# Kernel tuning notes

Measured on AMD Instinct MI355X. Metric: run time of the kernel, lower is better.

## Reference

```python
import jax, jax.numpy as jnp
import numpy as np

N_NODES = 50000


def gcn_conv(x, W, b, src, dst):
    # PyG GCNConv: h = x @ W; add self-loops; norm = deg^{-1/2}[src]*deg^{-1/2}[dst];
    # out = scatter_add(norm * h[src] -> dst) + bias
    h = x @ W  # [N, out]
    ones = jnp.ones(src.shape[0], dtype=x.dtype)
    deg = jax.ops.segment_sum(ones, dst, num_segments=N_NODES) + 1.0  # +1 for self-loop
    inv_sqrt = deg ** -0.5
    norm = inv_sqrt[src] * inv_sqrt[dst]  # [E]
    msgs = h[src] * norm[:, None]  # [E, out]
    agg = jax.ops.segment_sum(msgs, dst, num_segments=N_NODES)
    # self-loop contribution: norm_ii = deg_i^{-1}
    agg = agg + h * (inv_sqrt * inv_sqrt)[:, None]
    return agg + b


def setup_inputs() -> dict:
    key = jax.random.key(0)
    k1, k2, k3, k4 = jax.random.split(key, 4)
    d_in, d_h = 256, 256
    x = jax.random.normal(k1, (N_NODES, d_in), dtype=jnp.float32)
    edge_index = jax.random.randint(k2, (2, 800000), 0, N_NODES, dtype=jnp.int64)
    # Glorot-style params (GCNConv linear has no bias; separate bias added post-agg)
    W1 = jax.random.normal(k3, (d_in, d_h), dtype=jnp.float32) / np.sqrt(d_in)
    W2 = jax.random.normal(k4, (d_h, d_h), dtype=jnp.float32) / np.sqrt(d_h)
    b1 = jnp.zeros((d_h,), dtype=jnp.float32)
    b2 = jnp.zeros((d_h,), dtype=jnp.float32)
    return {"x": x, "edge_index": edge_index, "W1": W1, "b1": b1, "W2": W2, "b2": b2}


def reference(x, edge_index, W1, b1, W2, b2):
    src, dst = edge_index[0], edge_index[1]
    h = jax.nn.relu(gcn_conv(x, W1, b1, src, dst))
    h = jax.nn.relu(gcn_conv(h, W2, b2, src, dst))
    # global_mean_pool with batch=arange(N) assigns each node its own graph -> identity
    return h
```

## Files before the change

### kernel.cpp

```cpp
#include <hip/hip_runtime.h>
#include <hip/hip_bf16.h>

typedef unsigned short u16;
typedef unsigned int u32;

#define N_NODES 50000
#define N_EDGES 800000
#define DHID 256
#define ELLW 64

typedef __attribute__((ext_vector_type(8))) _Float16 f16x8;
typedef __attribute__((ext_vector_type(4))) float f32x4;
typedef __attribute__((ext_vector_type(2))) float f32x2;

__device__ __forceinline__ u16 f2bf(float f) {
    u32 u = __float_as_uint(f);
    u32 r = (u + 0x7FFFu + ((u >> 16) & 1u)) >> 16;
    return (u16)r;
}
__device__ __forceinline__ u16 f2h(float f) {
    _Float16 h = (_Float16)f;
    union { _Float16 h; u16 u; } c; c.h = h;
    return c.u;
}
__device__ __forceinline__ void gl_lds16(const void* g, void* l) {
    __builtin_amdgcn_global_load_lds(
        (const __attribute__((address_space(1))) u32*)g,
        (__attribute__((address_space(3))) u32*)l, 16, 0, 0);
}

#define SPLIT_BLKS 12500
#define ZERO_BLKS 196
__global__ void prep_fused(const float* __restrict__ x, u16* __restrict__ xf,
                           const float* __restrict__ W1, const float* __restrict__ W2,
                           u16* __restrict__ W1t, u16* __restrict__ W2t,
                           int* __restrict__ deg, u32* __restrict__ hszero) {
    const int b = blockIdx.x, tid = threadIdx.x;
    if (b < SPLIT_BLKS) {
        int i = b * 256 + tid;
        float4 v = ((const float4*)x)[i];
        u16 h0 = f2h(v.x), h1 = f2h(v.y), h2 = f2h(v.z), h3 = f2h(v.w);
        uint2 hv;
        hv.x = (u32)h0 | ((u32)h1 << 16);
        hv.y = (u32)h2 | ((u32)h3 << 16);
        ((uint2*)xf)[i] = hv;
    } else if (b < SPLIT_BLKS + ZERO_BLKS) {
        int j = (b - SPLIT_BLKS) * 256 + tid;
        if (j < N_NODES) deg[j] = 0;
        if (j < 128) hszero[j] = 0;
    } else {
        int idx = b - (SPLIT_BLKS + ZERO_BLKS);
        int y = idx >> 8, n = idx & 255, k = tid;
        const float* W = y ? W2 : W1;
        u16* o = y ? W2t : W1t;
        o[n * 256 + k] = f2h(W[k * 256 + n]);
    }
}

__global__ void fill_kernel(const int* __restrict__ src, const int* __restrict__ dst,
                            int* __restrict__ deg, u16* __restrict__ col16, int E) {
    int e = blockIdx.x * 256 + threadIdx.x;
    if (e < E) {
        int d = dst[e];
        int p = atomicAdd(&deg[d], 1);
        if (p < ELLW) col16[(size_t)d * ELLW + p] = (u16)src[e];
    }
}

__global__ __launch_bounds__(256) void gemm_f16_kernel(
    const u16* __restrict__ Af, const u16* __restrict__ Bt,
    const int* __restrict__ deg, u16* __restrict__ out, int M) {
    __shared__ u16 As[2][128 * 32];
    __shared__ u16 Bs[2][128 * 32];
    const int tid = threadIdx.x;
    const int wave = tid >> 6;
    const int lane = tid & 63;
    const int wm = wave >> 1, wn = wave & 1;
    const int quad = lane >> 4, l16 = lane & 15;
    const int m0 = blockIdx.x * 128;
    const int n0 = blockIdx.y * 128;

    f32x4 acc[4][4] = {};

    const int rl = tid >> 2;
    const int cl = tid & 3;
    const int kk = ((cl ^ (rl & 3) ^ ((rl >> 2) & 3)) & 3) * 8;
    int ar0 = m0 + rl; if (ar0 >= M) ar0 = M - 1;
    int ar1 = m0 + 64 + rl; if (ar1 >= M) ar1 = M - 1;
    const size_t aoff0 = (size_t)ar0 * 256 + kk;
    const size_t aoff1 = (size_t)ar1 * 256 + kk;
    const size_t boff0 = (size_t)(n0 + rl) * 256 + kk;
    const size_t boff1 = (size_t)(n0 + 64 + rl) * 256 + kk;
    const size_t l0 = (size_t)wave * 512;
    const size_t l1 = 2048 + (size_t)wave * 512;

    const int qs8 = ((quad ^ (l16 & 3) ^ ((l16 >> 2) & 3)) & 3) * 8;

#define STAGE(buf, ko)                                      \
    {                                                       \
        const int koff_ = (ko) * 32;                        \
        gl_lds16(Af + aoff0 + koff_, &As[buf][l0]);         \
        gl_lds16(Af + aoff1 + koff_, &As[buf][l1]);         \
        gl_lds16(Bt + boff0 + koff_, &Bs[buf][l0]);         \
        gl_lds16(Bt + boff1 + koff_, &Bs[buf][l1]);         \
    }

    STAGE(0, 0);
    asm volatile("s_waitcnt vmcnt(0)" ::: "memory");
    __syncthreads();

    int cur = 0;
    for (int ko = 0; ko < 8; ++ko) {
        if (ko < 7) STAGE(cur ^ 1, ko + 1);

        f16x8 af[4], bf[4];
#pragma unroll
        for (int mi = 0; mi < 4; ++mi)
            af[mi] = *(const f16x8*)&As[cur][(wm * 64 + mi * 16 + l16) * 32 + qs8];
#pragma unroll
        for (int ni = 0; ni < 4; ++ni)
            bf[ni] = *(const f16x8*)&Bs[cur][(wn * 64 + ni * 16 + l16) * 32 + qs8];
#pragma unroll
        for (int mi = 0; mi < 4; ++mi)
#pragma unroll
            for (int ni = 0; ni < 4; ++ni)
                acc[mi][ni] = __builtin_amdgcn_mfma_f32_16x16x32_f16(af[mi], bf[ni], acc[mi][ni], 0, 0, 0);

        if (ko < 7) {
            asm volatile("s_waitcnt vmcnt(0)" ::: "memory");
            __syncthreads();
            cur ^= 1;
        }
    }
#undef STAGE

#pragma unroll
    for (int mi = 0; mi < 4; ++mi) {
#pragma unroll
        for (int r = 0; r < 4; ++r) {
            int row = m0 + wm * 64 + mi * 16 + quad * 4 + r;
            if (row < M) {
                float s = rsqrtf((float)deg[row] + 1.0f);
#pragma unroll
                for (int ni = 0; ni < 4; ++ni) {
                    int c = n0 + wn * 64 + ni * 16 + l16;
                    out[(size_t)row * 256 + c] = f2bf(acc[mi][ni][r] * s);
                }
            }
        }
    }
}

__global__ __launch_bounds__(256) void agg_kernel(
    const u16* __restrict__ hs, const u16* __restrict__ col16,
    const int* __restrict__ deg, const float* __restrict__ bias,
    u16* __restrict__ out_f16, float* __restrict__ out_f,
    int mode, int Nn) {
    const int wave = threadIdx.x >> 6, lane = threadIdx.x & 63;
    const int i = blockIdx.x * 4 + wave;
    if (i >= Nn) return;

    const int cnt = deg[i];
    const size_t ebase = (size_t)i * ELLW;
    int entry = Nn;
    if (lane == 0) entry = i;
    else if (lane - 1 < cnt) entry = (int)col16[ebase + lane - 1];
    int entries = cnt + 1;
    if (entries > 64) entries = 64;
    const int nb = (entries + 3) >> 2;
    const size_t lofs = (size_t)lane * 4;

    f32x2 a01 = {0.f, 0.f}, a23 = {0.f, 0.f};

#define ISSUE(b, x0, x1, x2, x3)                                                \
    {                                                                           \
        int e0 = __builtin_amdgcn_readlane(entry, (b) * 4 + 0);                 \
        int e1 = __builtin_amdgcn_readlane(entry, (b) * 4 + 1);                 \
        int e2 = __builtin_amdgcn_readlane(entry, (b) * 4 + 2);                 \
        int e3 = __builtin_amdgcn_readlane(entry, (b) * 4 + 3);                 \
        x0 = *(const uint2*)(hs + (size_t)e0 * 256 + lofs);                     \
        x1 = *(const uint2*)(hs + (size_t)e1 * 256 + lofs);                     \
        x2 = *(const uint2*)(hs + (size_t)e2 * 256 + lofs);                     \
        x3 = *(const uint2*)(hs + (size_t)e3 * 256 + lofs);                     \
    }
#define ACCUM(v)                                                                \
    {                                                                           \
        f32x2 p0, p1;                                                           \
        p0.x = __uint_as_float(v.x << 16);                                      \
        p0.y = __uint_as_float(v.x & 0xffff0000u);                              \
        p1.x = __uint_as_float(v.y << 16);                                      \
        p1.y = __uint_as_float(v.y & 0xffff0000u);                              \
        a01 += p0; a23 += p1;                                                   \
    }

    uint2 c0, c1, c2, c3, d0, d1, d2, d3, n0v, n1v, n2v, n3v;
    ISSUE(0, c0, c1, c2, c3);
    if (nb > 1) ISSUE(1, d0, d1, d2, d3);
    for (int b = 0; b < nb; ++b) {
        const bool more2 = (b + 2 < nb);
        if (more2) ISSUE(b + 2, n0v, n1v, n2v, n3v);
        ACCUM(c0); ACCUM(c1); ACCUM(c2); ACCUM(c3);
        c0 = d0; c1 = d1; c2 = d2; c3 = d3;
        d0 = n0v; d1 = n1v; d2 = n2v; d3 = n3v;
    }
    {
        int cap = cnt < ELLW ? cnt : ELLW;
        for (int j = 63; j < cap; ++j) {
            int s = (int)col16[ebase + j];
            uint2 v = *(const uint2*)(hs + (size_t)s * 256 + lofs);
            ACCUM(v);
        }
    }
#undef ISSUE
#undef ACCUM

    const float inv = rsqrtf((float)cnt + 1.0f);
    float4 bb = *(const float4*)(bias + lane * 4);
    float r0 = fmaxf(fmaf(a01.x, inv, bb.x), 0.0f);
    float r1 = fmaxf(fmaf(a01.y, inv, bb.y), 0.0f);
    float r2 = fmaxf(fmaf(a23.x, inv, bb.z), 0.0f);
    float r3 = fmaxf(fmaf(a23.y, inv, bb.w), 0.0f);
    const size_t o = (size_t)i * 256 + lane * 4;
    if (mode == 0) {
        u16 h0 = f2h(r0), h1 = f2h(r1), h2 = f2h(r2), h3 = f2h(r3);
        uint2 w;
        w.x = (u32)h0 | ((u32)h1 << 16);
        w.y = (u32)h2 | ((u32)h3 << 16);
        *(uint2*)(out_f16 + o) = w;
    } else {
        *(float4*)(out_f + o) = make_float4(r0, r1, r2, r3);
    }
}

extern "C" void kernel_launch(void* const* d_in, const int* in_sizes, int n_in,
                              void* d_out, int out_size, void* d_ws, size_t ws_size,
                              hipStream_t stream) {
    const float* x = (const float*)d_in[0];
    const int* ei = (const int*)d_in[1];
    const float* W1 = (const float*)d_in[2];
    const float* b1 = (const float*)d_in[3];
    const float* W2 = (const float*)d_in[4];
    const float* b2 = (const float*)d_in[5];
    float* out = (float*)d_out;

    const int Nn = N_NODES, E = N_EDGES;
    const int* srcp = ei;
    const int* dstp = ei + E;

    u16* Af = (u16*)d_out;

    char* p = (char*)d_ws;
    auto take = [&](size_t bytes) -> void* {
        void* r = (void*)p;
        p += (bytes + 255) & ~(size_t)255;
        return r;
    };
    u16* hs    = (u16*)take((size_t)(Nn + 1) * DHID * 2);
    u16* col16 = (u16*)take((size_t)Nn * ELLW * 2);
    int* deg   = (int*)take((size_t)Nn * 4);
    u16* W1t   = (u16*)take(256 * 256 * 2);
    u16* W2t   = (u16*)take(256 * 256 * 2);

    prep_fused<<<SPLIT_BLKS + ZERO_BLKS + 512, 256, 0, stream>>>(
        x, Af, W1, W2, W1t, W2t, deg, (u32*)(hs + (size_t)Nn * DHID));
    fill_kernel<<<E / 256, 256, 0, stream>>>(srcp, dstp, deg, col16, E);

    const int gm = (Nn + 127) / 128;
    gemm_f16_kernel<<<dim3(gm, 2), 256, 0, stream>>>(Af, W1t, deg, hs, Nn);
    agg_kernel<<<(Nn + 3) / 4, 256, 0, stream>>>(hs, col16, deg, b1, Af, nullptr, 0, Nn);
    gemm_f16_kernel<<<dim3(gm, 2), 256, 0, stream>>>(Af, W2t, deg, hs, Nn);
    agg_kernel<<<(Nn + 3) / 4, 256, 0, stream>>>(hs, col16, deg, b2, nullptr, out, 1, Nn);
}
```

Baseline: 308.5 us.

## Slice hidden features into 32-column panels for cache-local aggregation

The GEMM now writes its bf16 output in a sliced layout: 8 slices of 32 columns, each a contiguous [N+1, 32] array. The aggregation kernel assigns each block to one slice and 16 nodes, so each gather reads 64-byte rows from a smaller working set that should fit better in cache. The zero-fill now runs as its own kernel, and the edge-fill work is merged into the prep kernel. One risk is that merging fill into prep lets the fill atomics run concurrently with other prep blocks. Another is that the aggregation loop becomes fully unrolled with shuffles, and each lane now issues narrower 4-byte loads.

```diff
diff --git a/kernel.cpp b/kernel.cpp
--- a/kernel.cpp
+++ b/kernel.cpp
@@ -8,10 +8,11 @@
 #define N_EDGES 800000
 #define DHID 256
 #define ELLW 64
+#define NSLICE 8
+#define SLICEW 32
 
 typedef __attribute__((ext_vector_type(8))) _Float16 f16x8;
 typedef __attribute__((ext_vector_type(4))) float f32x4;
-typedef __attribute__((ext_vector_type(2))) float f32x2;
 
 __device__ __forceinline__ u16 f2bf(float f) {
     u32 u = __float_as_uint(f);
@@ -29,12 +30,23 @@
         (__attribute__((address_space(3))) u32*)l, 16, 0, 0);
 }
 
+__global__ void zero_kernel(int* __restrict__ deg, u32* __restrict__ hss32) {
+    int j = blockIdx.x * 256 + threadIdx.x;
+    if (j < N_NODES) deg[j] = 0;
+    if (j < NSLICE * 16) {
+        int s = j >> 4, w = j & 15;
+        hss32[((size_t)s * (N_NODES + 1) + N_NODES) * 16 + w] = 0;
+    }
+}
+
 #define SPLIT_BLKS 12500
-#define ZERO_BLKS 196
-__global__ void prep_fused(const float* __restrict__ x, u16* __restrict__ xf,
-                           const float* __restrict__ W1, const float* __restrict__ W2,
-                           u16* __restrict__ W1t, u16* __restrict__ W2t,
-                           int* __restrict__ deg, u32* __restrict__ hszero) {
+#define W_BLKS 512
+#define FILL_BLKS 3125
+__global__ void prep_fill(const float* __restrict__ x, u16* __restrict__ xf,
+                          const float* __restrict__ W1, const float* __restrict__ W2,
+                          u16* __restrict__ W1t, u16* __restrict__ W2t,
+                          const int* __restrict__ src, const int* __restrict__ dst,
+                          int* __restrict__ deg, u16* __restrict__ col16) {
     const int b = blockIdx.x, tid = threadIdx.x;
     if (b < SPLIT_BLKS) {
         int i = b * 256 + tid;
@@ -44,23 +56,14 @@
         hv.x = (u32)h0 | ((u32)h1 << 16);
         hv.y = (u32)h2 | ((u32)h3 << 16);
         ((uint2*)xf)[i] = hv;
-    } else if (b < SPLIT_BLKS + ZERO_BLKS) {
-        int j = (b - SPLIT_BLKS) * 256 + tid;
-        if (j < N_NODES) deg[j] = 0;
-        if (j < 128) hszero[j] = 0;
-    } else {
-        int idx = b - (SPLIT_BLKS + ZERO_BLKS);
+    } else if (b < SPLIT_BLKS + W_BLKS) {
+        int idx = b - SPLIT_BLKS;
         int y = idx >> 8, n = idx & 255, k = tid;
         const float* W = y ? W2 : W1;
         u16* o = y ? W2t : W1t;
         o[n * 256 + k] = f2h(W[k * 256 + n]);
-    }
-}
-
-__global__ void fill_kernel(const int* __restrict__ src, const int* __restrict__ dst,
-                            int* __restrict__ deg, u16* __restrict__ col16, int E) {
-    int e = blockIdx.x * 256 + threadIdx.x;
-    if (e < E) {
+    } else {
+        int e = (b - SPLIT_BLKS - W_BLKS) * 256 + tid;
         int d = dst[e];
         int p = atomicAdd(&deg[d], 1);
         if (p < ELLW) col16[(size_t)d * ELLW + p] = (u16)src[e];
@@ -69,7 +72,7 @@
 
 __global__ __launch_bounds__(256) void gemm_f16_kernel(
     const u16* __restrict__ Af, const u16* __restrict__ Bt,
-    const int* __restrict__ deg, u16* __restrict__ out, int M) {
+    const int* __restrict__ deg, u16* __restrict__ hss, int M) {
     __shared__ u16 As[2][128 * 32];
     __shared__ u16 Bs[2][128 * 32];
     const int tid = threadIdx.x;
@@ -144,7 +147,8 @@
 #pragma unroll
                 for (int ni = 0; ni < 4; ++ni) {
                     int c = n0 + wn * 64 + ni * 16 + l16;
-                    out[(size_t)row * 256 + c] = f2bf(acc[mi][ni][r] * s);
+                    size_t o = ((size_t)(c >> 5) * (N_NODES + 1) + row) * 32 + (c & 31);
+                    hss[o] = f2bf(acc[mi][ni][r] * s);
                 }
             }
         }
@@ -152,83 +156,67 @@
 }
 
 __global__ __launch_bounds__(256) void agg_kernel(
-    const u16* __restrict__ hs, const u16* __restrict__ col16,
+    const u16* __restrict__ hss, const u16* __restrict__ col16,
     const int* __restrict__ deg, const float* __restrict__ bias,
     u16* __restrict__ out_f16, float* __restrict__ out_f,
     int mode, int Nn) {
+    const int slice = blockIdx.x & 7;
+    const int chunk = blockIdx.x >> 3;
     const int wave = threadIdx.x >> 6, lane = threadIdx.x & 63;
-    const int i = blockIdx.x * 4 + wave;
-    if (i >= Nn) return;
+    const int sg = lane >> 4, l16 = lane & 15;
+    const int i = chunk * 16 + wave * 4 + sg;
+    const u16* hsS = hss + (size_t)slice * (Nn + 1) * 32;
 
     const int cnt = deg[i];
     const size_t ebase = (size_t)i * ELLW;
-    int entry = Nn;
-    if (lane == 0) entry = i;
-    else if (lane - 1 < cnt) entry = (int)col16[ebase + lane - 1];
+    int eA = (l16 == 0) ? i : ((l16 - 1 < cnt) ? (int)col16[ebase + l16 - 1] : Nn);
+    int eB = (l16 + 15 < cnt) ? (int)col16[ebase + l16 + 15] : Nn;
+    int eC = (l16 + 31 < cnt) ? (int)col16[ebase + l16 + 31] : Nn;
+    int eD = (l16 + 47 < cnt) ? (int)col16[ebase + l16 + 47] : Nn;
     int entries = cnt + 1;
     if (entries > 64) entries = 64;
-    const int nb = (entries + 3) >> 2;
-    const size_t lofs = (size_t)lane * 4;
-
-    f32x2 a01 = {0.f, 0.f}, a23 = {0.f, 0.f};
-
-#define ISSUE(b, x0, x1, x2, x3)                                                \
+
+    float a0 = 0.f, a1 = 0.f;
+    const int lbase = sg * 16;
+    const int lofs = l16 * 2;
+
+#define BATCH(v, q)                                                             \
     {                                                                           \
-        int e0 = __builtin_amdgcn_readlane(entry, (b) * 4 + 0);                 \
-        int e1 = __builtin_amdgcn_readlane(entry, (b) * 4 + 1);                 \
-        int e2 = __builtin_amdgcn_readlane(entry, (b) * 4 + 2);                 \
-        int e3 = __builtin_amdgcn_readlane(entry, (b) * 4 + 3);                 \
-        x0 = *(const uint2*)(hs + (size_t)e0 * 256 + lofs);                     \
-        x1 = *(const uint2*)(hs + (size_t)e1 * 256 + lofs);                     \
-        x2 = *(const uint2*)(hs + (size_t)e2 * 256 + lofs);                     \
-        x3 = *(const uint2*)(hs + (size_t)e3 * 256 + lofs);                     \
-    }
-#define ACCUM(v)                                                                \
-    {                                                                           \
-        f32x2 p0, p1;                                                           \
-        p0.x = __uint_as_float(v.x << 16);                                      \
-        p0.y = __uint_as_float(v.x & 0xffff0000u);                              \
-        p1.x = __uint_as_float(v.y << 16);                                      \
-        p1.y = __uint_as_float(v.y & 0xffff0000u);                              \
-        a01 += p0; a23 += p1;                                                   \
-    }
-
-    uint2 c0, c1, c2, c3, d0, d1, d2, d3, n0v, n1v, n2v, n3v;
-    ISSUE(0, c0, c1, c2, c3);
-    if (nb > 1) ISSUE(1, d0, d1, d2, d3);
-    for (int b = 0; b < nb; ++b) {
-        const bool more2 = (b + 2 < nb);
-        if (more2) ISSUE(b + 2, n0v, n1v, n2v, n3v);
-        ACCUM(c0); ACCUM(c1); ACCUM(c2); ACCUM(c3);
-        c0 = d0; c1 = d1; c2 = d2; c3 = d3;
-        d0 = n0v; d1 = n1v; d2 = n2v; d3 = n3v;
-    }
-    {
-        int cap = cnt < ELLW ? cnt : ELLW;
-        for (int j = 63; j < cap; ++j) {
-            int s = (int)col16[ebase + j];
-            uint2 v = *(const uint2*)(hs + (size_t)s * 256 + lofs);
-            ACCUM(v);
+        int e0 = __shfl((v), lbase + (q) * 4 + 0, 64);                          \
+        int e1 = __shfl((v), lbase + (q) * 4 + 1, 64);                          \
+        int e2 = __shfl((v), lbase + (q) * 4 + 2, 64);                          \
+        int e3 = __shfl((v), lbase + (q) * 4 + 3, 64);                          \
+        u32 v0 = *(const u32*)(hsS + (size_t)e0 * 32 + lofs);                   \
+        u32 v1 = *(const u32*)(hsS + (size_t)e1 * 32 + lofs);                   \
+        u32 v2 = *(const u32*)(hsS + (size_t)e2 * 32 + lofs);                   \
+        u32 v3 = *(const u32*)(hsS + (size_t)e3 * 32 + lofs);                   \
+        a0 += __uint_as_float(v0 << 16);  a1 += __uint_as_float(v0 & 0xffff0000u); \
+        a0 += __uint_as_float(v1 << 16);  a1 += __uint_as_float(v1 & 0xffff0000u); \
+        a0 += __uint_as_float(v2 << 16);  a1 += __uint_as_float(v2 & 0xffff0000u); \
+        a0 += __uint_as_float(v3 << 16);  a1 += __uint_as_float(v3 & 0xffff0000u); \
+    }
+
+#pragma unroll
+    for (int r = 0; r < 4; ++r) {
+        int v = (r == 0) ? eA : (r == 1) ? eB : (r == 2) ? eC : eD;
+#pragma unroll
+        for (int q = 0; q < 4; ++q) {
+            int gs = r * 16 + q * 4;
+            if (gs < entries) BATCH(v, q);
         }
     }
-#undef ISSUE
-#undef ACCUM
+#undef BATCH
 
     const float inv = rsqrtf((float)cnt + 1.0f);
-    float4 bb = *(const float4*)(bias + lane * 4);
-    float r0 = fmaxf(fmaf(a01.x, inv, bb.x), 0.0f);
-    float r1 = fmaxf(fmaf(a01.y, inv, bb.y), 0.0f);
-    float r2 = fmaxf(fmaf(a23.x, inv, bb.z), 0.0f);
-    float r3 = fmaxf(fmaf(a23.y, inv, bb.w), 0.0f);
-    const size_t o = (size_t)i * 256 + lane * 4;
+    float2 bb = *(const float2*)(bias + slice * 32 + lofs);
+    float r0 = fmaxf(fmaf(a0, inv, bb.x), 0.0f);
+    float r1 = fmaxf(fmaf(a1, inv, bb.y), 0.0f);
+    const size_t o = (size_t)i * 256 + slice * 32 + lofs;
     if (mode == 0) {
-        u16 h0 = f2h(r0), h1 = f2h(r1), h2 = f2h(r2), h3 = f2h(r3);
-        uint2 w;
-        w.x = (u32)h0 | ((u32)h1 << 16);
-        w.y = (u32)h2 | ((u32)h3 << 16);
-        *(uint2*)(out_f16 + o) = w;
+        u32 w = (u32)f2h(r0) | ((u32)f2h(r1) << 16);
+        *(u32*)(out_f16 + o) = w;
     } else {
-        *(float4*)(out_f + o) = make_float4(r0, r1, r2, r3);
+        *(float2*)(out_f + o) = make_float2(r0, r1);
     }
 }
 
@@ -255,19 +243,20 @@
         p += (bytes + 255) & ~(size_t)255;
         return r;
     };
-    u16* hs    = (u16*)take((size_t)(Nn + 1) * DHID * 2);
+    u16* hss   = (u16*)take((size_t)NSLICE * (Nn + 1) * SLICEW * 2);
     u16* col16 = (u16*)take((size_t)Nn * ELLW * 2);
     int* deg   = (int*)take((size_t)Nn * 4);
     u16* W1t   = (u16*)take(256 * 256 * 2);
     u16* W2t   = (u16*)take(256 * 256 * 2);
 
-    prep_fused<<<SPLIT_BLKS + ZERO_BLKS + 512, 256, 0, stream>>>(
-        x, Af, W1, W2, W1t, W2t, deg, (u32*)(hs + (size_t)Nn * DHID));
-    fill_kernel<<<E / 256, 256, 0, stream>>>(srcp, dstp, deg, col16, E);
+    zero_kernel<<<196, 256, 0, stream>>>(deg, (u32*)hss);
+    prep_fill<<<SPLIT_BLKS + W_BLKS + FILL_BLKS, 256, 0, stream>>>(
+        x, Af, W1, W2, W1t, W2t, srcp, dstp, deg, col16);
 
     const int gm = (Nn + 127) / 128;
-    gemm_f16_kernel<<<dim3(gm, 2), 256, 0, stream>>>(Af, W1t, deg, hs, Nn);
-    agg_kernel<<<(Nn + 3) / 4, 256, 0, stream>>>(hs, col16, deg, b1, Af, nullptr, 0, Nn);
-    gemm_f16_kernel<<<dim3(gm, 2), 256, 0, stream>>>(Af, W2t, deg, hs, Nn);
-    agg_kernel<<<(Nn + 3) / 4, 256, 0, stream>>>(hs, col16, deg, b2, nullptr, out, 1, Nn);
-}
+    const int ga = (Nn / 16) * NSLICE;
+    gemm_f16_kernel<<<dim3(gm, 2), 256, 0, stream>>>(Af, W1t, deg, hss, Nn);
+    agg_kernel<<<ga, 256, 0, stream>>>(hss, col16, deg, b1, Af, nullptr, 0, Nn);
+    gemm_f16_kernel<<<dim3(gm, 2), 256, 0, stream>>>(Af, W2t, deg, hss, Nn);
+    agg_kernel<<<ga, 256, 0, stream>>>(hss, col16, deg, b2, nullptr, out, 1, Nn);
+}
```

New measurement: 324.0 us. 1.05x slower.
